# Performance work log

Measured on AMD Instinct MI355X. Metric: run time of the kernel, lower is better.

The kernel has to match this reference:

```python
import jax, jax.numpy as jnp
import numpy as np

E = 250000   # n_scanned_edges
B = 16       # batch_size
N = 50000    # n_entities (n_nodes)
R = 500      # n_relations
D_IN = 100   # input embedding dim (proj input)
D = 64       # n_dims_sm
M = 2 * E    # n_memorized_and_scanned_nodes (>= n_vi_groups + n_vj_groups)


def setup_inputs() -> dict:
    rng = np.random.default_rng(0)
    eg = rng.integers(0, B, E)
    vi = rng.integers(0, N, E)
    vj = rng.integers(0, N, E)
    order = np.lexsort((vj, vi, eg))  # sorted by (eg_idx, vi, vj) as the module assumes
    eg, vi, vj = eg[order], vi[order], vj[order]
    rel = rng.integers(0, R, E)
    # dense group ids; idx_vi is non-decreasing because edges are lexsorted by (eg,vi)
    idx_vi = np.unique(eg.astype(np.int64) * N + vi, return_inverse=True)[1]
    idx_vj = np.unique(eg.astype(np.int64) * N + vj, return_inverse=True)[1]
    n_vi = int(idx_vi.max()) + 1
    edges = np.stack([eg, vi, vj, rel, idx_vi, idx_vj, idx_vi, n_vi + idx_vj], 1).astype(np.int32)

    key = jax.random.key(0)
    ks = jax.random.split(key, 24)
    nrm = lambda k, shp, s=1.0: jax.random.normal(k, shp, jnp.float32) * s
    na = jax.random.uniform(ks[0], (B, N), jnp.float32)
    na = na / jnp.sum(na, 1, keepdims=True)  # node attention is a distribution per example
    inp = {
        "node_attention": na,
        "scanned_edges": jnp.asarray(edges),
        "hidden_uncon": nrm(ks[1], (1, N, D_IN)),
        "hidden_con": nrm(ks[2], (M, D_IN)),
        "rel_table": nrm(ks[3], (R, D_IN)),
        "query_head_emb": nrm(ks[4], (B, D_IN)),
        "query_rel_emb": nrm(ks[5], (B, D_IN)),
        "p_W": nrm(ks[6], (D_IN, D), 0.1),
        "p_b": jnp.zeros((D,), jnp.float32),
    }
    i = 7
    for g in ("g1", "g2"):
        for nm, shp in (("lW", (4 * D, D)), ("lb", (D,)), ("rW", (4 * D, D)), ("rb", (D,)), ("cW", (D, D)), ("cb", (D,))):
            inp[g + "_" + nm] = nrm(ks[i], shp, 0.05)
            i += 1
    return inp


def _g(left, right, lW, lb, rW, rb, cW, cb):
    # G layer: sum(left_dense(cat(left)) * center_dense(right_dense(cat(right))), -1)
    lx = jnp.concatenate(left, -1)
    rx = jnp.concatenate(right, -1)
    l = jax.nn.leaky_relu(lx @ lW + lb, 0.2)  # tf.nn.leaky_relu alpha=0.2
    r = jax.nn.leaky_relu(rx @ rW + rb, 0.2)
    return jnp.sum(l * (r @ cW + cb), -1)


def reference(node_attention, scanned_edges, hidden_uncon, hidden_con, rel_table,
              query_head_emb, query_rel_emb, p_W, p_b,
              g1_lW, g1_lb, g1_rW, g1_rb, g1_cW, g1_cb,
              g2_lW, g2_lb, g2_rW, g2_rb, g2_cW, g2_cb):
    Bn, Nn = node_attention.shape
    En = scanned_edges.shape[0]
    proj = lambda x: jnp.tanh(x @ p_W + p_b)

    h_con = proj(hidden_con)       # (M, D)
    h_uncon = proj(hidden_uncon)   # (1, N, D)
    qh = proj(query_head_emb)      # (B, D)
    qr = proj(query_rel_emb)

    e = scanned_edges
    eg, vi, vj = e[:, 0], e[:, 1], e[:, 2]
    idx_vi = e[:, 4]
    # node2edge gathers
    h_vi = h_con[e[:, 6]]          # (E, D)
    h_vj = h_con[e[:, 7]]
    hu_vj = h_uncon[0][vj]         # hidden_uncon batch is 1 -> idx 0
    remb = proj(rel_table[e[:, 3]])
    qhv = qh[eg]
    qrv = qr[eg]

    left = (h_vi, remb, qhv, qrv)
    logits = _g(left, (h_vj, remb, qhv, qrv), g1_lW, g1_lb, g1_rW, g1_rb, g1_cW, g1_cb)
    logits = logits + _g(left, (hu_vj, remb, qhv, qrv), g2_lW, g2_lb, g2_rW, g2_rb, g2_cW, g2_cb)

    # neighbor softmax over sorted idx_vi segments
    m = jax.ops.segment_max(logits, idx_vi, num_segments=En, indices_are_sorted=True)
    ex = jnp.exp(logits - m[idx_vi])
    den = jax.ops.segment_sum(ex, idx_vi, num_segments=En, indices_are_sorted=True)
    transition = ex / den[idx_vi]

    # flow attention: gather at (eg, vi), scatter-sum at (eg, vj)
    trans_att = node_attention[eg, vi] * transition
    new_att = jnp.zeros((Bn, Nn), node_attention.dtype).at[eg, vj].add(trans_att)
    new_att = new_att / jnp.sum(new_att, axis=1, keepdims=True)
    return new_att
```

## Files before the change

### kernel.cpp

```cpp
#include <hip/hip_runtime.h>

#define DIN 100
#define DD  64
#define NE  250000
#define NB  16
#define NN  50000
#define NR  500
#define NM  500000
#define NH  (NM + NN)

#define H_OFF    64
#define TA2_OFF  (H_OFF + NH*DD)
#define RT_OFF   (TA2_OFF + NE*DD)
#define QT_OFF   (RT_OFF + 4*NR*DD)
#define LG_OFF   (QT_OFF + 4*NB*DD)

#define PA 320
#define PB 160
#define PC 32

#define XT_STRIDE 260

#define PCHUNK  20
#define NPCHUNK 5

__device__ __forceinline__ void fma4x4(const float4 x, const float4 w, float4 acc[4]) {
  acc[0].x += x.x*w.x; acc[0].y += x.x*w.y; acc[0].z += x.x*w.z; acc[0].w += x.x*w.w;
  acc[1].x += x.y*w.x; acc[1].y += x.y*w.y; acc[1].z += x.y*w.z; acc[1].w += x.y*w.w;
  acc[2].x += x.z*w.x; acc[2].y += x.z*w.y; acc[2].z += x.z*w.z; acc[2].w += x.z*w.w;
  acc[3].x += x.w*w.x; acc[3].y += x.w*w.y; acc[3].z += x.w*w.z; acc[3].w += x.w*w.w;
}

__device__ __forceinline__ float4 leaky4(float4 v) {
  v.x = v.x > 0.f ? v.x : 0.2f*v.x;
  v.y = v.y > 0.f ? v.y : 0.2f*v.y;
  v.z = v.z > 0.f ? v.z : 0.2f*v.z;
  v.w = v.w > 0.f ? v.w : 0.2f*v.w;
  return v;
}

__global__ void k_init(int* wsI, float* bsum) {
  if (threadIdx.x == 0) { wsI[0] = 0x7fffffff; wsI[1] = 0; }
  if (threadIdx.x < NB) bsum[threadIdx.x] = 0.f;
}

__global__ void k_limits(const int* __restrict__ edges, int* __restrict__ wsI) {
  int i = blockIdx.x * blockDim.x + threadIdx.x;
  int mn = 0x7fffffff, mx = -1;
  if (i < NE) { int v = edges[i*8 + 7]; mn = v; mx = v; }
  for (int off = 32; off > 0; off >>= 1) {
    mn = min(mn, __shfl_down(mn, off));
    mx = max(mx, __shfl_down(mx, off));
  }
  if ((threadIdx.x & 63) == 0) {
    atomicMin(&wsI[0], mn);
    atomicMax(&wsI[1], mx + 1);
  }
}

__global__ void k_tables(const float* __restrict__ rtab,
                         const float* __restrict__ qh, const float* __restrict__ qr,
                         const float* __restrict__ pW, const float* __restrict__ pb,
                         const float* __restrict__ g1_lW, const float* __restrict__ g1_lb,
                         const float* __restrict__ g1_rW, const float* __restrict__ g1_rb,
                         const float* __restrict__ g2_lW, const float* __restrict__ g2_lb,
                         const float* __restrict__ g2_rW, const float* __restrict__ g2_rb,
                         float* __restrict__ rT, float* __restrict__ qT) {
  __shared__ float xs[DIN], xs2[DIN], ps[DD], ps2[DD];
  const int d = threadIdx.x;
  const int blk = blockIdx.x;
  if (blk < NR) {
    for (int k = d; k < DIN; k += 64) xs[k] = rtab[blk*DIN + k];
    __syncthreads();
    float a = pb[d];
    for (int k = 0; k < DIN; ++k) a += xs[k] * pW[k*DD + d];
    ps[d] = tanhf(a);
    __syncthreads();
    float o1 = 0.f, o2 = 0.f, o3 = 0.f, o4 = 0.f;
    for (int k = 0; k < DD; ++k) {
      float p = ps[k];
      o1 += p * g1_lW[(DD + k)*DD + d];
      o2 += p * g1_rW[(DD + k)*DD + d];
      o3 += p * g2_lW[(DD + k)*DD + d];
      o4 += p * g2_rW[(DD + k)*DD + d];
    }
    rT[(0*NR + blk)*DD + d] = o1;
    rT[(1*NR + blk)*DD + d] = o2;
    rT[(2*NR + blk)*DD + d] = o3;
    rT[(3*NR + blk)*DD + d] = o4;
  } else {
    const int b = blk - NR;
    for (int k = d; k < DIN; k += 64) { xs[k] = qh[b*DIN + k]; xs2[k] = qr[b*DIN + k]; }
    __syncthreads();
    float a = pb[d], a2 = pb[d];
    for (int k = 0; k < DIN; ++k) { a += xs[k]*pW[k*DD + d]; a2 += xs2[k]*pW[k*DD + d]; }
    ps[d] = tanhf(a); ps2[d] = tanhf(a2);
    __syncthreads();
    float o1 = g1_lb[d], o2 = g1_rb[d], o3 = g2_lb[d], o4 = g2_rb[d];
    for (int k = 0; k < DD; ++k) {
      float p = ps[k], p2 = ps2[k];
      o1 += p * g1_lW[(2*DD + k)*DD + d] + p2 * g1_lW[(3*DD + k)*DD + d];
      o2 += p * g1_rW[(2*DD + k)*DD + d] + p2 * g1_rW[(3*DD + k)*DD + d];
      o3 += p * g2_lW[(2*DD + k)*DD + d] + p2 * g2_lW[(3*DD + k)*DD + d];
      o4 += p * g2_rW[(2*DD + k)*DD + d] + p2 * g2_rW[(3*DD + k)*DD + d];
    }
    qT[(0*NB + b)*DD + d] = o1;
    qT[(1*NB + b)*DD + d] = o2;
    qT[(2*NB + b)*DD + d] = o3;
    qT[(3*NB + b)*DD + d] = o4;
  }
}

__global__ __launch_bounds__(256, 2)
void k_proj(const float* __restrict__ hcon, const float* __restrict__ huncon,
            const float* __restrict__ pW, const float* __restrict__ pb,
            const int* __restrict__ lim, float* __restrict__ H) {
  __shared__ __align__(16) float pWs[DIN*DD];
  __shared__ __align__(16) float Xt[PCHUNK][XT_STRIDE];
  const int tid = threadIdx.x;
  for (int i = tid; i < DIN*DD; i += 256) pWs[i] = pW[i];
  const int tc = tid & 7, tr = tid >> 3;
  const int c0 = tc << 3;
  const float4 pb0 = *(const float4*)&pb[c0];
  const float4 pb1 = *(const float4*)&pb[c0 + 4];
  const int nmax = lim[1];
  const int t_lo = (nmax + 255) >> 8;
  const int NT   = t_lo + ((NN + 255) >> 8);
  __syncthreads();
  for (int t = blockIdx.x; t < NT; t += gridDim.x) {
    const int row0 = (t < t_lo) ? (t << 8) : (NM + ((t - t_lo) << 8));
    const int myrow = row0 + tid;
    const float* src = nullptr;
    if (myrow < NH) src = (myrow < NM) ? &hcon[(size_t)myrow*DIN]
                                       : &huncon[(size_t)(myrow - NM)*DIN];
    float4 acc[2][2][4];
    #pragma unroll
    for (int a = 0; a < 2; ++a)
      #pragma unroll
      for (int b = 0; b < 2; ++b)
        #pragma unroll
        for (int i = 0; i < 4; ++i) acc[a][b][i] = make_float4(0.f,0.f,0.f,0.f);
    for (int ch = 0; ch < NPCHUNK; ++ch) {
      const int kb = ch * PCHUNK;
      __syncthreads();
      if (src) {
        #pragma unroll
        for (int j = 0; j < PCHUNK; j += 4) {
          float4 v = *(const float4*)&src[kb + j];
          Xt[j+0][tid] = v.x; Xt[j+1][tid] = v.y; Xt[j+2][tid] = v.z; Xt[j+3][tid] = v.w;
        }
      }
      __syncthreads();
      for (int k = 0; k < PCHUNK; ++k) {
        float4 x0 = *(const float4*)&Xt[k][tr*8];
        float4 x1 = *(const float4*)&Xt[k][tr*8 + 4];
        float4 w0 = *(const float4*)&pWs[(kb + k)*DD + c0];
        float4 w1 = *(const float4*)&pWs[(kb + k)*DD + c0 + 4];
        fma4x4(x0, w0, acc[0][0]); fma4x4(x0, w1, acc[0][1]);
        fma4x4(x1, w0, acc[1][0]); fma4x4(x1, w1, acc[1][1]);
      }
    }
    #pragma unroll
    for (int a = 0; a < 2; ++a)
      #pragma unroll
      for (int i = 0; i < 4; ++i) {
        int row = row0 + tr*8 + a*4 + i;
        if (row < NH) {
          float4 o0, o1;
          o0.x = tanhf(acc[a][0][i].x + pb0.x);
          o0.y = tanhf(acc[a][0][i].y + pb0.y);
          o0.z = tanhf(acc[a][0][i].z + pb0.z);
          o0.w = tanhf(acc[a][0][i].w + pb0.w);
          o1.x = tanhf(acc[a][1][i].x + pb1.x);
          o1.y = tanhf(acc[a][1][i].y + pb1.y);
          o1.z = tanhf(acc[a][1][i].z + pb1.z);
          o1.w = tanhf(acc[a][1][i].w + pb1.w);
          *(float4*)&H[row*DD + c0]     = o0;
          *(float4*)&H[row*DD + c0 + 4] = o1;
        }
      }
  }
}

__global__ __launch_bounds__(256, 2)
void k_tf(const float* __restrict__ g1_lW, const float* __restrict__ g1_rW,
          const float* __restrict__ g2_lW, const float* __restrict__ g2_rW,
          const int* __restrict__ lim,
          float* __restrict__ H, float* __restrict__ TA2) {
  __shared__ __align__(16) float Ws0[DD*DD];
  __shared__ __align__(16) float Ws1[DD*DD];
  __shared__ __align__(16) float Ht[32][XT_STRIDE];
  const int tid = threadIdx.x;
  const int nvi  = lim[0];
  const int nmax = lim[1];
  int pool, pbase, pgrid;
  if (blockIdx.x < PA)           { pool = 0; pbase = blockIdx.x;           pgrid = PA; }
  else if (blockIdx.x < PA + PB) { pool = 1; pbase = blockIdx.x - PA;      pgrid = PB; }
  else                           { pool = 2; pbase = blockIdx.x - PA - PB; pgrid = PC; }
  if (pool == 0) {
    for (int i = tid; i < DD*DD; i += 256) { Ws0[i] = g1_lW[i]; Ws1[i] = g2_lW[i]; }
  } else if (pool == 1) {
    for (int i = tid; i < DD*DD; i += 256) Ws0[i] = g1_rW[i];
  } else {
    for (int i = tid; i < DD*DD; i += 256) Ws0[i] = g2_rW[i];
  }
  int t_begin, t_count, row_base;
  if (pool == 0)      { t_begin = 0;        t_count = (nvi + 255) >> 8;                 row_base = 0;  }
  else if (pool == 1) { t_begin = nvi >> 8; t_count = ((nmax + 255) >> 8) - (nvi >> 8); row_base = 0;  }
  else                { t_begin = 0;        t_count = (NN + 255) >> 8;                  row_base = NM; }
  const int tc = tid & 7, tr = tid >> 3;
  const int c0 = tc << 3;
  __syncthreads();
  for (int tt = pbase; tt < t_count; tt += pgrid) {
    const int row0 = row_base + ((t_begin + tt) << 8);
    const int myrow = row0 + tid;
    float4 a0[2][2][4], a1[2][2][4];
    #pragma unroll
    for (int a = 0; a < 2; ++a)
      #pragma unroll
      for (int b = 0; b < 2; ++b)
        #pragma unroll
        for (int i = 0; i < 4; ++i) {
          a0[a][b][i] = make_float4(0.f,0.f,0.f,0.f);
          a1[a][b][i] = make_float4(0.f,0.f,0.f,0.f);
        }
    #pragma unroll
    for (int chunk = 0; chunk < 2; ++chunk) {
      const int kb = chunk << 5;
      __syncthreads();
      if (myrow < NH) {
        const float* src = &H[(size_t)myrow*DD + kb];
        #pragma unroll
        for (int j = 0; j < 32; j += 4) {
          float4 v = *(const float4*)&src[j];
          Ht[j+0][tid] = v.x; Ht[j+1][tid] = v.y; Ht[j+2][tid] = v.z; Ht[j+3][tid] = v.w;
        }
      }
      __syncthreads();
      if (pool == 0) {
        for (int k = 0; k < 32; ++k) {
          float4 x0 = *(const float4*)&Ht[k][tr*8];
          float4 x1 = *(const float4*)&Ht[k][tr*8 + 4];
          float4 w0 = *(const float4*)&Ws0[(kb + k)*DD + c0];
          float4 w1 = *(const float4*)&Ws0[(kb + k)*DD + c0 + 4];
          float4 u0 = *(const float4*)&Ws1[(kb + k)*DD + c0];
          float4 u1 = *(const float4*)&Ws1[(kb + k)*DD + c0 + 4];
          fma4x4(x0, w0, a0[0][0]); fma4x4(x0, w1, a0[0][1]);
          fma4x4(x1, w0, a0[1][0]); fma4x4(x1, w1, a0[1][1]);
          fma4x4(x0, u0, a1[0][0]); fma4x4(x0, u1, a1[0][1]);
          fma4x4(x1, u0, a1[1][0]); fma4x4(x1, u1, a1[1][1]);
        }
      } else {
        for (int k = 0; k < 32; ++k) {
          float4 x0 = *(const float4*)&Ht[k][tr*8];
          float4 x1 = *(const float4*)&Ht[k][tr*8 + 4];
          float4 w0 = *(const float4*)&Ws0[(kb + k)*DD + c0];
          float4 w1 = *(const float4*)&Ws0[(kb + k)*DD + c0 + 4];
          fma4x4(x0, w0, a0[0][0]); fma4x4(x0, w1, a0[0][1]);
          fma4x4(x1, w0, a0[1][0]); fma4x4(x1, w1, a0[1][1]);
        }
      }
    }
    #pragma unroll
    for (int a = 0; a < 2; ++a)
      #pragma unroll
      for (int i = 0; i < 4; ++i) {
        int row = row0 + tr*8 + a*4 + i;
        bool ok;
        if (pool == 0)      ok = (row < nvi);
        else if (pool == 1) ok = (row >= nvi && row < nmax);
        else                ok = (row < NH);
        if (ok) {
          *(float4*)&H[row*DD + c0]     = a0[a][0][i];
          *(float4*)&H[row*DD + c0 + 4] = a0[a][1][i];
          if (pool == 0) {
            *(float4*)&TA2[row*DD + c0]     = a1[a][0][i];
            *(float4*)&TA2[row*DD + c0 + 4] = a1[a][1][i];
          }
        }
      }
  }
}

__global__ __launch_bounds__(256, 2)
void k_edges(const int* __restrict__ edges,
             const float* __restrict__ TA, const float* __restrict__ TA2,
             const float* __restrict__ HU2,
             const float* __restrict__ rT, const float* __restrict__ qT,
             const float* __restrict__ cW1, const float* __restrict__ cb1,
             const float* __restrict__ cW2, const float* __restrict__ cb2,
             float* __restrict__ logits) {
  __shared__ __align__(16) float Wt1s[DD*68];
  __shared__ __align__(16) float Wt2s[DD*68];
  __shared__ __align__(16) float Lt[DD][68];
  __shared__ __align__(16) float Rt[DD][68];
  __shared__ __align__(16) float4 cbs4[2][16];
  __shared__ float lg[64];
  __shared__ int   se[64*8];
  const int tid = threadIdx.x;
  for (int i = tid; i < DD*DD; i += 256) {
    int k = i >> 6, d = i & 63;
    Wt1s[d*68 + k] = cW1[i];
    Wt2s[d*68 + k] = cW2[i];
  }
  if (tid < 16) {
    cbs4[0][tid] = *(const float4*)&cb1[tid*4];
    cbs4[1][tid] = *(const float4*)&cb2[tid*4];
  }
  const int e   = tid >> 2;
  const int d0  = (tid & 3) * 16;
  const int ee0 = (tid & 15) << 2;
  const int k0  = (tid >> 4) << 2;
  __syncthreads();
  const int NT = (NE + 63) / 64;
  for (int tile = blockIdx.x; tile < NT; tile += gridDim.x) {
    const int e0 = tile * 64;
    const int ecnt = min(64, NE - e0);
    for (int i = tid; i < 64*8; i += 256) se[i] = (i < ecnt*8) ? edges[e0*8 + i] : 0;
    if (tid < 64) lg[tid] = 0.f;
    __syncthreads();
    const int rel = se[e*8 + 3];
    const int eg  = se[e*8 + 0];
    const int li  = se[e*8 + 6];
    for (int g = 0; g < 2; ++g) {
      const float* Lb = g ? TA2 : TA;
      const float* Rb = g ? HU2 : TA;
      const float* rL = rT + (g ? 2*NR*DD : 0);
      const float* rR = rT + (g ? 3*NR*DD : 1*NR*DD);
      const float* qL = qT + (g ? 2*NB*DD : 0);
      const float* qR = qT + (g ? 3*NB*DD : 1*NB*DD);
      const float* Wts = g ? Wt2s : Wt1s;
      const int ri = g ? se[e*8 + 2] : se[e*8 + 7];
      float cbp = 0.f;
      #pragma unroll
      for (int di = 0; di < 4; ++di) {
        const int d = d0 + 4*di;
        float4 l = *(const float4*)&Lb[li*DD + d];
        float4 t = *(const float4*)&rL[rel*DD + d];
        float4 u = *(const float4*)&qL[eg*DD + d];
        l.x += t.x + u.x; l.y += t.y + u.y; l.z += t.z + u.z; l.w += t.w + u.w;
        l = leaky4(l);
        Lt[d+0][e] = l.x; Lt[d+1][e] = l.y; Lt[d+2][e] = l.z; Lt[d+3][e] = l.w;
        float4 c = cbs4[g][d >> 2];
        cbp += l.x*c.x + l.y*c.y + l.z*c.z + l.w*c.w;
        float4 r = *(const float4*)&Rb[ri*DD + d];
        t = *(const float4*)&rR[rel*DD + d];
        u = *(const float4*)&qR[eg*DD + d];
        r.x += t.x + u.x; r.y += t.y + u.y; r.z += t.z + u.z; r.w += t.w + u.w;
        r = leaky4(r);
        Rt[d+0][e] = r.x; Rt[d+1][e] = r.y; Rt[d+2][e] = r.z; Rt[d+3][e] = r.w;
      }
      atomicAdd(&lg[e], cbp);
      __syncthreads();
      float4 z[4] = {{0,0,0,0},{0,0,0,0},{0,0,0,0},{0,0,0,0}};
      for (int d = 0; d < DD; ++d) {
        float4 x = *(const float4*)&Lt[d][ee0];
        float4 w = *(const float4*)&Wts[d*68 + k0];
        fma4x4(x, w, z);
      }
      {
        float4 r0v = *(const float4*)&Rt[k0+0][ee0];
        float4 r1v = *(const float4*)&Rt[k0+1][ee0];
        float4 r2v = *(const float4*)&Rt[k0+2][ee0];
        float4 r3v = *(const float4*)&Rt[k0+3][ee0];
        float p0 = z[0].x*r0v.x + z[0].y*r1v.x + z[0].z*r2v.x + z[0].w*r3v.x;
        float p1 = z[1].x*r0v.y + z[1].y*r1v.y + z[1].z*r2v.y + z[1].w*r3v.y;
        float p2 = z[2].x*r0v.z + z[2].y*r1v.z + z[2].z*r2v.z + z[2].w*r3v.z;
        float p3 = z[3].x*r0v.w + z[3].y*r1v.w + z[3].z*r2v.w + z[3].w*r3v.w;
        atomicAdd(&lg[ee0+0], p0);
        atomicAdd(&lg[ee0+1], p1);
        atomicAdd(&lg[ee0+2], p2);
        atomicAdd(&lg[ee0+3], p3);
      }
      __syncthreads();
    }
    if (tid < ecnt) logits[e0 + tid] = lg[tid];
    __syncthreads();
  }
}

__global__ void k_softmax(const int* __restrict__ edges, const float* __restrict__ logits,
                          const float* __restrict__ na, float* __restrict__ out) {
  int e = blockIdx.x * blockDim.x + threadIdx.x;
  if (e >= NE) return;
  int seg = edges[e*8 + 4];
  if (e > 0 && edges[(e-1)*8 + 4] == seg) return;
  int j = e;
  float m = -1e30f;
  while (j < NE && edges[j*8 + 4] == seg) { m = fmaxf(m, logits[j]); ++j; }
  float s = 0.f;
  for (int t = e; t < j; ++t) s += expf(logits[t] - m);
  int eg = edges[e*8 + 0], vi = edges[e*8 + 1];
  float scale = na[eg*NN + vi] / s;
  for (int t = e; t < j; ++t) {
    int vj = edges[t*8 + 2];
    __hip_atomic_fetch_add(&out[eg*NN + vj], expf(logits[t] - m) * scale,
                           __ATOMIC_RELAXED, __HIP_MEMORY_SCOPE_AGENT);
  }
}

__global__ void k_rowsum(const float* __restrict__ out, float* __restrict__ bsum) {
  int b = blockIdx.y;
  float s = 0.f;
  for (int n = blockIdx.x * blockDim.x + threadIdx.x; n < NN; n += gridDim.x * blockDim.x)
    s += out[b*NN + n];
  for (int off = 32; off > 0; off >>= 1) s += __shfl_down(s, off);
  if ((threadIdx.x & 63) == 0)
    __hip_atomic_fetch_add(&bsum[b], s, __ATOMIC_RELAXED, __HIP_MEMORY_SCOPE_AGENT);
}

__global__ void k_div(float* __restrict__ out, const float* __restrict__ bsum) {
  int i = blockIdx.x * blockDim.x + threadIdx.x;
  if (i < NB*NN) out[i] /= bsum[i / NN];
}

extern "C" void kernel_launch(void* const* d_in, const int* in_sizes, int n_in,
                              void* d_out, int out_size, void* d_ws, size_t ws_size,
                              hipStream_t stream) {
  (void)in_sizes; (void)n_in; (void)out_size; (void)ws_size;
  const float* na     = (const float*)d_in[0];
  const int*   edges  = (const int*)  d_in[1];
  const float* huncon = (const float*)d_in[2];
  const float* hcon   = (const float*)d_in[3];
  const float* rtab   = (const float*)d_in[4];
  const float* qh     = (const float*)d_in[5];
  const float* qr     = (const float*)d_in[6];
  const float* pW     = (const float*)d_in[7];
  const float* pb     = (const float*)d_in[8];
  const float* g1_lW  = (const float*)d_in[9];
  const float* g1_lb  = (const float*)d_in[10];
  const float* g1_rW  = (const float*)d_in[11];
  const float* g1_rb  = (const float*)d_in[12];
  const float* g1_cW  = (const float*)d_in[13];
  const float* g1_cb  = (const float*)d_in[14];
  const float* g2_lW  = (const float*)d_in[15];
  const float* g2_lb  = (const float*)d_in[16];
  const float* g2_rW  = (const float*)d_in[17];
  const float* g2_rb  = (const float*)d_in[18];
  const float* g2_cW  = (const float*)d_in[19];
  const float* g2_cb  = (const float*)d_in[20];
  float* out  = (float*)d_out;
  float* ws   = (float*)d_ws;
  int*   wsI  = (int*)d_ws;
  float* bsum = ws + 16;
  float* H    = ws + H_OFF;
  float* TA2  = ws + TA2_OFF;
  float* rT   = ws + RT_OFF;
  float* qT   = ws + QT_OFF;
  float* lgp  = ws + LG_OFF;

  hipMemsetAsync(d_out, 0, (size_t)NB*NN*sizeof(float), stream);
  k_init<<<1, 64, 0, stream>>>(wsI, bsum);
  k_limits<<<(NE + 255)/256, 256, 0, stream>>>(edges, wsI);
  k_tables<<<NR + NB, 64, 0, stream>>>(rtab, qh, qr, pW, pb,
                                       g1_lW, g1_lb, g1_rW, g1_rb,
                                       g2_lW, g2_lb, g2_rW, g2_rb, rT, qT);
  k_proj<<<768, 256, 0, stream>>>(hcon, huncon, pW, pb, wsI, H);
  k_tf<<<PA + PB + PC, 256, 0, stream>>>(g1_lW, g1_rW, g2_lW, g2_rW, wsI, H, TA2);
  k_edges<<<512, 256, 0, stream>>>(edges, H, TA2, H + NM*DD, rT, qT,
                                   g1_cW, g1_cb, g2_cW, g2_cb, lgp);
  k_softmax<<<(NE + 255)/256, 256, 0, stream>>>(edges, lgp, na, out);
  k_rowsum<<<dim3(32, 16), 256, 0, stream>>>(out, bsum);
  k_div<<<(NB*NN + 255)/256, 256, 0, stream>>>(out, bsum);
}
```

Before: 815.1 us.

## Double-buffer projection tiles with async global-to-LDS loads and swizzled layout

The projection kernel now works on 64-row tiles instead of 256-row tiles. Each tile is staged directly into LDS with the global_load_lds builtin, using an XOR-swizzled row layout, and two buffers are used so the next tile loads while the current one is computed. This replaces the per-chunk register-to-LDS transpose and its repeated barriers, aiming to overlap memory traffic with the FMA work. In exchange each thread computes a 4x4 output block instead of 8x8, which gives less register reuse per LDS read. LDS use per block rises, which could limit occupancy.

```diff
diff --git a/kernel.cpp b/kernel.cpp
--- a/kernel.cpp
+++ b/kernel.cpp
@@ -21,8 +21,7 @@
 
 #define XT_STRIDE 260
 
-#define PCHUNK  20
-#define NPCHUNK 5
+#define PROJ_LDSF (64*104)
 
 __device__ __forceinline__ void fma4x4(const float4 x, const float4 w, float4 acc[4]) {
   acc[0].x += x.x*w.x; acc[0].y += x.x*w.y; acc[0].z += x.x*w.z; acc[0].w += x.x*w.w;
@@ -116,70 +115,100 @@
             const float* __restrict__ pW, const float* __restrict__ pb,
             const int* __restrict__ lim, float* __restrict__ H) {
   __shared__ __align__(16) float pWs[DIN*DD];
-  __shared__ __align__(16) float Xt[PCHUNK][XT_STRIDE];
-  const int tid = threadIdx.x;
+  __shared__ __align__(16) float Xb[2][PROJ_LDSF];
+  const int tid  = threadIdx.x;
   for (int i = tid; i < DIN*DD; i += 256) pWs[i] = pW[i];
-  const int tc = tid & 7, tr = tid >> 3;
-  const int c0 = tc << 3;
-  const float4 pb0 = *(const float4*)&pb[c0];
-  const float4 pb1 = *(const float4*)&pb[c0 + 4];
+  const int lane = tid & 63, wid = tid >> 6;
+  const int tc = tid & 15, tr = tid >> 4;
+  const int c0 = tc << 2, r0 = tr << 2;
+  const float4 pbv = *(const float4*)&pb[c0];
   const int nmax = lim[1];
-  const int t_lo = (nmax + 255) >> 8;
-  const int NT   = t_lo + ((NN + 255) >> 8);
+  const int tA = (nmax + 63) >> 6;
+  const int tB = (NN + 63) >> 6;
+  const int NT = tA + tB;
+  const int key = tr & 7;
+
+#define STAGE_TILE(T, BUF)                                                      \
+  {                                                                             \
+    const float* sbase; int rbase, rlim;                                        \
+    if ((T) < tA) { sbase = hcon;   rbase = (T) << 6;        rlim = NM; }       \
+    else          { sbase = huncon; rbase = ((T) - tA) << 6; rlim = NN; }       \
+    _Pragma("unroll")                                                           \
+    for (int j = 0; j < 7; ++j) {                                               \
+      int ii = j*4 + wid;                                                       \
+      if (ii < 26) {                                                            \
+        int p16  = ii*64 + lane;                                                \
+        int row  = p16 / 26;                                                    \
+        int slot = p16 - row*26;                                                \
+        int kk4  = (slot < 24) ? (slot ^ ((row >> 2) & 7)) : 24;                \
+        int grow = rbase + row; if (grow >= rlim) grow = rlim - 1;              \
+        const float* gp = sbase + (size_t)grow*DIN + kk4*4;                     \
+        __builtin_amdgcn_global_load_lds(                                       \
+            (const __attribute__((address_space(1))) void*)gp,                  \
+            (__attribute__((address_space(3))) void*)(&Xb[(BUF)][0] + ii*256),  \
+            16, 0, 0);                                                          \
+      }                                                                         \
+    }                                                                           \
+  }
+
+  {
+    int t0 = blockIdx.x;
+    if (t0 < NT) STAGE_TILE(t0, 0);
+  }
   __syncthreads();
-  for (int t = blockIdx.x; t < NT; t += gridDim.x) {
-    const int row0 = (t < t_lo) ? (t << 8) : (NM + ((t - t_lo) << 8));
-    const int myrow = row0 + tid;
-    const float* src = nullptr;
-    if (myrow < NH) src = (myrow < NM) ? &hcon[(size_t)myrow*DIN]
-                                       : &huncon[(size_t)(myrow - NM)*DIN];
-    float4 acc[2][2][4];
+
+  int it = 0;
+  for (int t = blockIdx.x; t < NT; t += gridDim.x, ++it) {
+    const int buf = it & 1;
+    const int tn = t + gridDim.x;
+    if (tn < NT) STAGE_TILE(tn, buf ^ 1);
+
+    float4 acc[4];
     #pragma unroll
-    for (int a = 0; a < 2; ++a)
-      #pragma unroll
-      for (int b = 0; b < 2; ++b)
-        #pragma unroll
-        for (int i = 0; i < 4; ++i) acc[a][b][i] = make_float4(0.f,0.f,0.f,0.f);
-    for (int ch = 0; ch < NPCHUNK; ++ch) {
-      const int kb = ch * PCHUNK;
-      __syncthreads();
-      if (src) {
-        #pragma unroll
-        for (int j = 0; j < PCHUNK; j += 4) {
-          float4 v = *(const float4*)&src[kb + j];
-          Xt[j+0][tid] = v.x; Xt[j+1][tid] = v.y; Xt[j+2][tid] = v.z; Xt[j+3][tid] = v.w;
-        }
-      }
-      __syncthreads();
-      for (int k = 0; k < PCHUNK; ++k) {
-        float4 x0 = *(const float4*)&Xt[k][tr*8];
-        float4 x1 = *(const float4*)&Xt[k][tr*8 + 4];
-        float4 w0 = *(const float4*)&pWs[(kb + k)*DD + c0];
-        float4 w1 = *(const float4*)&pWs[(kb + k)*DD + c0 + 4];
-        fma4x4(x0, w0, acc[0][0]); fma4x4(x0, w1, acc[0][1]);
-        fma4x4(x1, w0, acc[1][0]); fma4x4(x1, w1, acc[1][1]);
-      }
-    }
+    for (int i = 0; i < 4; ++i) acc[i] = make_float4(0.f, 0.f, 0.f, 0.f);
+
+    const float* Xp = &Xb[buf][0];
+    for (int k4 = 0; k4 < 25; ++k4) {
+      const int slot = (k4 < 24) ? (k4 ^ key) : 24;
+      float4 xa0 = *(const float4*)&Xp[(r0 + 0)*104 + slot*4];
+      float4 xa1 = *(const float4*)&Xp[(r0 + 1)*104 + slot*4];
+      float4 xa2 = *(const float4*)&Xp[(r0 + 2)*104 + slot*4];
+      float4 xa3 = *(const float4*)&Xp[(r0 + 3)*104 + slot*4];
+      const float* wb = &pWs[k4*4*DD + c0];
+      {
+        float4 w = *(const float4*)&wb[0*DD];
+        fma4x4(make_float4(xa0.x, xa1.x, xa2.x, xa3.x), w, acc);
+      }
+      {
+        float4 w = *(const float4*)&wb[1*DD];
+        fma4x4(make_float4(xa0.y, xa1.y, xa2.y, xa3.y), w, acc);
+      }
+      {
+        float4 w = *(const float4*)&wb[2*DD];
+        fma4x4(make_float4(xa0.z, xa1.z, xa2.z, xa3.z), w, acc);
+      }
+      {
+        float4 w = *(const float4*)&wb[3*DD];
+        fma4x4(make_float4(xa0.w, xa1.w, xa2.w, xa3.w), w, acc);
+      }
+    }
+
+    const int row0 = (t < tA) ? (t << 6) : (NM + ((t - tA) << 6));
     #pragma unroll
-    for (int a = 0; a < 2; ++a)
-      #pragma unroll
-      for (int i = 0; i < 4; ++i) {
-        int row = row0 + tr*8 + a*4 + i;
-        if (row < NH) {
-          float4 o0, o1;
-          o0.x = tanhf(acc[a][0][i].x + pb0.x);
-          o0.y = tanhf(acc[a][0][i].y + pb0.y);
-          o0.z = tanhf(acc[a][0][i].z + pb0.z);
-          o0.w = tanhf(acc[a][0][i].w + pb0.w);
-          o1.x = tanhf(acc[a][1][i].x + pb1.x);
-          o1.y = tanhf(acc[a][1][i].y + pb1.y);
-          o1.z = tanhf(acc[a][1][i].z + pb1.z);
-          o1.w = tanhf(acc[a][1][i].w + pb1.w);
-          *(float4*)&H[row*DD + c0]     = o0;
-          *(float4*)&H[row*DD + c0 + 4] = o1;
-        }
-      }
-  }
+    for (int i = 0; i < 4; ++i) {
+      int row = row0 + r0 + i;
+      if (row < NH) {
+        float4 o;
+        o.x = tanhf(acc[i].x + pbv.x);
+        o.y = tanhf(acc[i].y + pbv.y);
+        o.z = tanhf(acc[i].z + pbv.z);
+        o.w = tanhf(acc[i].w + pbv.w);
+        *(float4*)&H[(size_t)row*DD + c0] = o;
+      }
+    }
+    __syncthreads();
+  }
+#undef STAGE_TILE
 }
 
 __global__ __launch_bounds__(256, 2)
```

New measurement: 807.7 us. Within noise of the previous version (-0.9%).
